# Kernel optimization log

Hardware: AMD Instinct MI355X
Metric: run time of the kernel (lower is better)

The kernel has to match this reference:

```python
import jax, jax.numpy as jnp
import numpy as np

NFEAT, NHID, NCLASS = 256, 128, 40
N_NODES, N_EDGES = 50000, 800000
BN_EPS = 1e-5


def setup_inputs() -> dict:
    key = jax.random.key(0)
    ks = jax.random.split(key, 8)
    x = jax.random.normal(ks[0], (N_NODES, NFEAT), dtype=jnp.float32)
    edge_index = jax.random.randint(ks[1], (2, N_EDGES), 0, N_NODES, dtype=jnp.int64)
    # GCNConv layer 0: nfeat -> nhid (Glorot-ish scale)
    W0 = jax.random.normal(ks[2], (NFEAT, NHID), dtype=jnp.float32) / np.sqrt(NFEAT)
    b0 = jnp.zeros((NHID,), dtype=jnp.float32)
    # BatchNorm1d(nhid)
    gamma0 = jnp.ones((NHID,), dtype=jnp.float32)
    beta0 = jnp.zeros((NHID,), dtype=jnp.float32)
    # GCNConv last: nhid -> nclass
    W1 = jax.random.normal(ks[3], (NHID, NCLASS), dtype=jnp.float32) / np.sqrt(NHID)
    b1 = jnp.zeros((NCLASS,), dtype=jnp.float32)
    return {"x": x, "edge_index": edge_index, "W0": W0, "b0": b0,
            "gamma0": gamma0, "beta0": beta0, "W1": W1, "b1": b1}


def _gcn_conv(x, src, dst, W, b, num_nodes):
    # normalize=False GCNConv: linear transform then raw sum aggregation src->dst
    h = x @ W                                   # [N, out]
    out = jax.ops.segment_sum(h[src], dst, num_segments=num_nodes)
    return out + b


def reference(x, edge_index, W0, b0, gamma0, beta0, W1, b1):
    N = x.shape[0]
    src, dst = edge_index[0], edge_index[1]
    # layer 0 conv
    h = _gcn_conv(x, src, dst, W0, b0, N)       # [N, nhid]
    # BatchNorm1d (training-mode batch stats, biased variance)
    mu = h.mean(axis=0)
    var = jnp.mean((h - mu) ** 2, axis=0)
    h = gamma0 * (h - mu) * jax.lax.rsqrt(var + BN_EPS) + beta0
    h = jax.nn.relu(h)
    # (dropout skipped: deterministic eval baseline)
    # last conv (early-return path in original forward)
    out = _gcn_conv(h, src, dst, W1, b1, N)     # [N, nclass]
    return out
```

## Files before the change

kernel.cpp:

```cpp
#include <hip/hip_runtime.h>

#define NFEAT 256
#define NHID 128
#define NCLASS 40
#define NNODES 50000
#define NEDGES 800000
#define BN_EPS 1e-5f
#define NBK 196
#define NBLK 100
#define EPB 8000
#define BKCAP 6144
#define NW1 6250
#define GEMM1_BLOCKS 1563

typedef __attribute__((ext_vector_type(4))) float f32x4;
typedef __attribute__((ext_vector_type(8))) short bf16x8;

__device__ inline ushort f2bf(float f) {
    uint u = __float_as_uint(f);
    u += 0x7FFF + ((u >> 16) & 1);
    return (ushort)(u >> 16);
}
__device__ inline float bflo(uint v) { return __uint_as_float(v << 16); }
__device__ inline float bfhi(uint v) { return __uint_as_float(v & 0xFFFF0000u); }

__global__ void k_prep(const float* __restrict__ W0, ushort* __restrict__ W0F,
                       const int* __restrict__ ei, int* __restrict__ bcnt) {
    __shared__ int cnt[NBK];
    if (blockIdx.x < 16) {
        const int t = blockIdx.x * 256 + threadIdx.x;
        const int lane = t & 63;
        const int grp = t >> 6;
        const int kc = grp & 7, fi = grp >> 3;
        const int n = fi * 16 + (lane & 15);
        const int k0 = kc * 32 + (lane >> 4) * 8;
        ushort v[8];
        #pragma unroll
        for (int j = 0; j < 8; ++j) v[j] = f2bf(W0[(k0 + j) * NHID + n]);
        uint4 u;
        u.x = (uint)v[0] | ((uint)v[1] << 16);
        u.y = (uint)v[2] | ((uint)v[3] << 16);
        u.z = (uint)v[4] | ((uint)v[5] << 16);
        u.w = (uint)v[6] | ((uint)v[7] << 16);
        *(uint4*)&W0F[(grp * 64 + lane) * 8] = u;
    } else {
        const int blk = blockIdx.x - 16;
        const int t = threadIdx.x;
        if (t < NBK) cnt[t] = 0;
        __syncthreads();
        const int base = blk * EPB;
        for (int i = t; i < EPB; i += 256)
            atomicAdd(&cnt[ei[NEDGES + base + i] >> 8], 1);
        __syncthreads();
        if (t < NBK) bcnt[blk * NBK + t] = cnt[t];
    }
}

__global__ void k_bkscan(const int* __restrict__ bcnt, int* __restrict__ off,
                         int* __restrict__ bstart, int* __restrict__ rowptr,
                         float* __restrict__ stats) {
    __shared__ int tot[NBK];
    __shared__ int bs[NBK + 1];
    const int t = threadIdx.x;
    if (t < 256) stats[t] = 0.f;
    if (t < NBK) {
        int s = 0;
        for (int b = 0; b < NBLK; ++b) s += bcnt[b * NBK + t];
        tot[t] = s;
    }
    __syncthreads();
    if (t == 0) {
        int run = 0;
        for (int i = 0; i < NBK; ++i) { bs[i] = run; run += tot[i]; }
        bs[NBK] = run;
        rowptr[NNODES] = NEDGES;
    }
    __syncthreads();
    if (t <= NBK) bstart[t] = bs[t];
    if (t < NBK) {
        int run = bs[t];
        for (int b = 0; b < NBLK; ++b) { off[b * NBK + t] = run; run += bcnt[b * NBK + t]; }
    }
}

__launch_bounds__(256, 4)
__global__ void k_scatter_gemm1(const int* __restrict__ ei, const int* __restrict__ off,
                                uint* __restrict__ packed,
                                const float* __restrict__ x, const ushort* __restrict__ W0F,
                                ushort* __restrict__ h1) {
    __shared__ int cur[NBK];
    if (blockIdx.x < NBLK) {
        const int t = threadIdx.x, blk = blockIdx.x;
        if (t < NBK) cur[t] = off[blk * NBK + t];
        __syncthreads();
        const int base = blk * EPB;
        for (int i = t; i < EPB; i += 256) {
            const int src = ei[base + i];
            const int dst = ei[NEDGES + base + i];
            const int pos = atomicAdd(&cur[dst >> 8], 1);
            packed[pos] = (uint)src | ((uint)(dst & 255) << 16);
        }
    } else {
        const int gt = (blockIdx.x - NBLK) * 256 + threadIdx.x;
        const int w = gt >> 6;
        if (w >= NW1) return;
        const int lane = gt & 63;
        const int half = w & 1;
        const int node = (w >> 1) * 16 + (lane & 15);
        const int nclamp = node < NNODES ? node : NNODES - 1;
        const float* xg = &x[(long)nclamp * NFEAT + (lane >> 4) * 8];

        bf16x8 xf[8];
        #pragma unroll
        for (int kc = 0; kc < 8; ++kc) {
            const float4 a = *(const float4*)(xg + kc * 32);
            const float4 b = *(const float4*)(xg + kc * 32 + 4);
            xf[kc][0]=(short)f2bf(a.x); xf[kc][1]=(short)f2bf(a.y);
            xf[kc][2]=(short)f2bf(a.z); xf[kc][3]=(short)f2bf(a.w);
            xf[kc][4]=(short)f2bf(b.x); xf[kc][5]=(short)f2bf(b.y);
            xf[kc][6]=(short)f2bf(b.z); xf[kc][7]=(short)f2bf(b.w);
        }

        f32x4 acc[4];
        #pragma unroll
        for (int f = 0; f < 4; ++f) acc[f] = (f32x4){0.f, 0.f, 0.f, 0.f};

        const ushort* wbase = &W0F[(size_t)lane * 8];
        #pragma unroll
        for (int kc = 0; kc < 8; ++kc) {
            #pragma unroll
            for (int f = 0; f < 4; ++f) {
                const int grp = (half * 4 + f) * 8 + kc;
                const bf16x8 wf = *(const bf16x8*)&wbase[(size_t)grp * 64 * 8];
                acc[f] = __builtin_amdgcn_mfma_f32_16x16x32_bf16(wf, xf[kc], acc[f], 0, 0, 0);
            }
        }

        if (node < NNODES) {
            const int nq = (lane >> 4) * 4;
            ushort* hp = &h1[(long)node * NHID + half * 64 + nq];
            #pragma unroll
            for (int f = 0; f < 4; ++f) {
                uint lo = (uint)f2bf(acc[f][0]) | ((uint)f2bf(acc[f][1]) << 16);
                uint hi = (uint)f2bf(acc[f][2]) | ((uint)f2bf(acc[f][3]) << 16);
                *(uint2*)&hp[f * 16] = make_uint2(lo, hi);
            }
        }
    }
}

__launch_bounds__(256)
__global__ void k_bksort(const uint* __restrict__ packed, const int* __restrict__ bstart,
                         int* __restrict__ esrc, int* __restrict__ rowptr) {
    __shared__ uint pr[BKCAP];
    __shared__ int cnt[256], sc[256], cur[256];
    const int t = threadIdx.x, b = blockIdx.x;
    const int nb = bstart[b], ne = bstart[b + 1];
    const int n = ne - nb;
    cnt[t] = 0;
    __syncthreads();
    for (int i = t; i < n; i += 256) {
        const uint p = packed[nb + i];
        pr[i] = p;
        atomicAdd(&cnt[p >> 16], 1);
    }
    __syncthreads();
    const int v = cnt[t];
    sc[t] = v;
    __syncthreads();
    for (int o = 1; o < 256; o <<= 1) {
        const int tmp = (t >= o) ? sc[t - o] : 0;
        __syncthreads();
        sc[t] += tmp;
        __syncthreads();
    }
    const int excl = sc[t] - v;
    cur[t] = excl;
    const int node = (b << 8) + t;
    if (node < NNODES) rowptr[node] = nb + excl;
    __syncthreads();
    for (int i = t; i < n; i += 256) {
        const uint p = pr[i];
        const int pos = atomicAdd(&cur[p >> 16], 1);
        esrc[nb + pos] = (int)(p & 0xFFFFu);
    }
}

__launch_bounds__(256)
__global__ void k_gather1(const int* __restrict__ rowptr, const int* __restrict__ esrc,
                          const ushort* __restrict__ h1, const float* __restrict__ b0,
                          float* __restrict__ agg1) {
    const int w = (blockIdx.x * blockDim.x + threadIdx.x) >> 6;
    const int lane = threadIdx.x & 63;
    if (w >= NNODES) return;
    const int beg = rowptr[w], end = rowptr[w + 1];
    const int f = lane * 2;
    float2 acc = *(const float2*)&b0[f];
    int i = beg;
    for (; i + 7 < end; i += 8) {
        uint v[8];
        #pragma unroll
        for (int j = 0; j < 8; ++j)
            v[j] = *(const uint*)&h1[(long)esrc[i + j] * NHID + f];
        #pragma unroll
        for (int j = 0; j < 8; ++j) { acc.x += bflo(v[j]); acc.y += bfhi(v[j]); }
    }
    for (; i < end; ++i) {
        const uint v = *(const uint*)&h1[(long)esrc[i] * NHID + f];
        acc.x += bflo(v); acc.y += bfhi(v);
    }
    *(float2*)&agg1[(long)w * NHID + f] = acc;
}

__global__ void k_bnstats(const float* __restrict__ agg1,
                          float* __restrict__ sums, float* __restrict__ sumsq) {
    __shared__ float sd[256 * 4], sd2[256 * 4];
    const int t = threadIdx.x;
    const int c4 = (t & 31) * 4;
    const int rr = t >> 5;
    float4 s = make_float4(0.f,0.f,0.f,0.f), s2 = s;
    for (int r = blockIdx.x * 8 + rr; r < NNODES; r += gridDim.x * 8) {
        const float4 v = *(const float4*)&agg1[(long)r * NHID + c4];
        s.x += v.x; s.y += v.y; s.z += v.z; s.w += v.w;
        s2.x += v.x*v.x; s2.y += v.y*v.y; s2.z += v.z*v.z; s2.w += v.w*v.w;
    }
    *(float4*)&sd[t * 4] = s; *(float4*)&sd2[t * 4] = s2;
    __syncthreads();
    if (t < 32) {
        #pragma unroll
        for (int j = 1; j < 8; ++j) {
            const float4 a = *(const float4*)&sd[(j * 32 + t) * 4];
            const float4 a2 = *(const float4*)&sd2[(j * 32 + t) * 4];
            s = *(float4*)&sd[t * 4];
            s2 = *(float4*)&sd2[t * 4];
            s.x += a.x; s.y += a.y; s.z += a.z; s.w += a.w;
            s2.x += a2.x; s2.y += a2.y; s2.z += a2.z; s2.w += a2.w;
            *(float4*)&sd[t * 4] = s; *(float4*)&sd2[t * 4] = s2;
        }
        atomicAdd(&sums[c4 + 0], s.x);  atomicAdd(&sums[c4 + 1], s.y);
        atomicAdd(&sums[c4 + 2], s.z);  atomicAdd(&sums[c4 + 3], s.w);
        atomicAdd(&sumsq[c4 + 0], s2.x); atomicAdd(&sumsq[c4 + 1], s2.y);
        atomicAdd(&sumsq[c4 + 2], s2.z); atomicAdd(&sumsq[c4 + 3], s2.w);
    }
}

__launch_bounds__(256)
__global__ void k_gemm2(const float* __restrict__ agg1, const float* __restrict__ W1,
                        const float* __restrict__ sums, const float* __restrict__ sumsq,
                        const float* __restrict__ gamma, const float* __restrict__ beta,
                        ushort* __restrict__ h2) {
    __shared__ float xs[64 * 132];
    __shared__ float wt[40 * 132];
    __shared__ float s_scale[128], s_shift[128];
    const int t = threadIdx.x;
    const int base = blockIdx.x * 64;

    if (t < NHID) {
        const float mu = sums[t] * (1.f / NNODES);
        float var = sumsq[t] * (1.f / NNODES) - mu * mu;
        var = fmaxf(var, 0.f);
        const float sc = gamma[t] * rsqrtf(var + BN_EPS);
        s_scale[t] = sc;
        s_shift[t] = beta[t] - mu * sc;
    }
    for (int idx = t; idx < NHID * NCLASS; idx += 256) {
        const int c = idx / NCLASS, j = idx % NCLASS;
        wt[j * 132 + c] = W1[idx];
    }
    __syncthreads();
    {
        const int cc = (t & 31) * 4;
        const float4 sc = *(const float4*)&s_scale[cc];
        const float4 sh = *(const float4*)&s_shift[cc];
        const int rb = t >> 5;
        #pragma unroll
        for (int p = 0; p < 8; ++p) {
            const int row = p * 8 + rb;
            const int g = base + row;
            float4 v = make_float4(0.f, 0.f, 0.f, 0.f);
            if (g < NNODES) {
                const float4 a = *(const float4*)&agg1[(long)g * NHID + cc];
                v.x = fmaxf(a.x * sc.x + sh.x, 0.f);
                v.y = fmaxf(a.y * sc.y + sh.y, 0.f);
                v.z = fmaxf(a.z * sc.z + sh.z, 0.f);
                v.w = fmaxf(a.w * sc.w + sh.w, 0.f);
            }
            *(float4*)&xs[row * 132 + cc] = v;
        }
    }
    __syncthreads();

    const int node = t >> 2;
    const int j0 = (t & 3) * 10;
    float acc[10] = {};
    for (int c4 = 0; c4 < 32; ++c4) {
        const int c = c4 * 4;
        const float4 a = *(const float4*)&xs[node * 132 + c];
        #pragma unroll
        for (int jj = 0; jj < 10; ++jj) {
            const float4 wv = *(const float4*)&wt[(j0 + jj) * 132 + c];
            acc[jj] += a.x * wv.x + a.y * wv.y + a.z * wv.z + a.w * wv.w;
        }
    }
    const int g = base + node;
    if (g < NNODES) {
        #pragma unroll
        for (int p = 0; p < 5; ++p) {
            uint u = (uint)f2bf(acc[2 * p]) | ((uint)f2bf(acc[2 * p + 1]) << 16);
            *(uint*)&h2[(long)g * NCLASS + j0 + 2 * p] = u;
        }
    }
}

__launch_bounds__(256)
__global__ void k_gather2(const int* __restrict__ rowptr, const int* __restrict__ esrc,
                          const ushort* __restrict__ h2, const float* __restrict__ b1,
                          float* __restrict__ out) {
    const int t = threadIdx.x;
    if (t >= 240) return;
    const int node = blockIdx.x * 12 + t / 20;
    if (node >= NNODES) return;
    const int f = (t % 20) * 2;
    const int beg = rowptr[node], end = rowptr[node + 1];
    float2 acc = make_float2(b1[f], b1[f + 1]);
    int i = beg;
    for (; i + 3 < end; i += 4) {
        const uint v0 = *(const uint*)&h2[(long)esrc[i]     * NCLASS + f];
        const uint v1 = *(const uint*)&h2[(long)esrc[i + 1] * NCLASS + f];
        const uint v2 = *(const uint*)&h2[(long)esrc[i + 2] * NCLASS + f];
        const uint v3 = *(const uint*)&h2[(long)esrc[i + 3] * NCLASS + f];
        acc.x += (bflo(v0) + bflo(v1)) + (bflo(v2) + bflo(v3));
        acc.y += (bfhi(v0) + bfhi(v1)) + (bfhi(v2) + bfhi(v3));
    }
    for (; i < end; ++i) {
        const uint v = *(const uint*)&h2[(long)esrc[i] * NCLASS + f];
        acc.x += bflo(v); acc.y += bfhi(v);
    }
    *(float2*)&out[(long)node * NCLASS + f] = acc;
}

extern "C" void kernel_launch(void* const* d_in, const int* in_sizes, int n_in,
                              void* d_out, int out_size, void* d_ws, size_t ws_size,
                              hipStream_t stream) {
    const float* x      = (const float*)d_in[0];
    const int*   ei     = (const int*)d_in[1];
    const float* W0     = (const float*)d_in[2];
    const float* b0     = (const float*)d_in[3];
    const float* gamma0 = (const float*)d_in[4];
    const float* beta0  = (const float*)d_in[5];
    const float* W1     = (const float*)d_in[6];
    const float* b1     = (const float*)d_in[7];
    float* out = (float*)d_out;

    char* ws = (char*)d_ws;
    float* sums  = (float*)ws;
    float* sumsq = sums + 128;
    int* wsI     = (int*)(ws + 4096);
    int* rowptr  = wsI;
    int* esrc    = wsI + 50048;
    int* bcnt    = wsI + 850048;
    int* off     = wsI + 869696;
    int* bstart  = wsI + 889344;
    ushort* W0F  = (ushort*)(ws + 3563520);
    ushort* h1   = (ushort*)(ws + 3629056);
    float* agg1  = (float*)(ws + 16429056);
    uint* packed = (uint*)agg1;
    ushort* h2   = h1;

    k_prep<<<16 + NBLK, 256, 0, stream>>>(W0, W0F, ei, bcnt);
    k_bkscan<<<1, 256, 0, stream>>>(bcnt, off, bstart, rowptr, sums);
    k_scatter_gemm1<<<NBLK + GEMM1_BLOCKS, 256, 0, stream>>>(ei, off, packed, x, W0F, h1);
    k_bksort<<<NBK, 256, 0, stream>>>(packed, bstart, esrc, rowptr);
    k_gather1<<<(NNODES * 64 + 255) / 256, 256, 0, stream>>>(rowptr, esrc, h1, b0, agg1);
    k_bnstats<<<256, 256, 0, stream>>>(agg1, sums, sumsq);
    k_gemm2<<<(NNODES + 63) / 64, 256, 0, stream>>>(agg1, W1, sums, sumsq, gamma0, beta0, h2);
    k_gather2<<<(NNODES + 11) / 12, 256, 0, stream>>>(rowptr, esrc, h2, b1, out);
}
```

Baseline: 176.2 us.

## Store layer-1 hidden features as FP8, parallelize bucket scan, batch x loads

The layer-1 hidden features h1 are now stored as packed FP8 e4m3 instead of bf16, which halves the bytes the edge gather reads per edge. The serial bucket prefix sum in k_bkscan is replaced by a parallel shared-memory scan. The GEMM1 path now issues all x loads before converting them, and its launch-bounds occupancy hint is removed. FP8 storage loses precision on the hidden activations, which may push results outside tolerance.

```diff
diff --git a/kernel.cpp b/kernel.cpp
--- a/kernel.cpp
+++ b/kernel.cpp
@@ -1,4 +1,5 @@
 #include <hip/hip_runtime.h>
+#include <hip/hip_fp8.h>
 
 #define NFEAT 256
 #define NHID 128
@@ -24,6 +25,32 @@
 __device__ inline float bflo(uint v) { return __uint_as_float(v << 16); }
 __device__ inline float bfhi(uint v) { return __uint_as_float(v & 0xFFFF0000u); }
 
+__device__ inline uint pk_fp8x4(float a0, float a1, float a2, float a3) {
+#if __has_builtin(__builtin_amdgcn_cvt_pk_fp8_f32)
+    int u = 0;
+    u = __builtin_amdgcn_cvt_pk_fp8_f32(a0, a1, u, false);
+    u = __builtin_amdgcn_cvt_pk_fp8_f32(a2, a3, u, true);
+    return (uint)u;
+#else
+    __hip_fp8_e4m3 q0(a0), q1(a1), q2(a2), q3(a3);
+    return (uint)q0.__x | ((uint)q1.__x << 8) | ((uint)q2.__x << 16) | ((uint)q3.__x << 24);
+#endif
+}
+__device__ inline float fp8lo(uint v) {
+#if __has_builtin(__builtin_amdgcn_cvt_f32_fp8)
+    return __builtin_amdgcn_cvt_f32_fp8((int)v, 0);
+#else
+    __hip_fp8_e4m3 q; q.__x = (__hip_fp8_storage_t)(v & 0xFF); return (float)q;
+#endif
+}
+__device__ inline float fp8hi(uint v) {
+#if __has_builtin(__builtin_amdgcn_cvt_f32_fp8)
+    return __builtin_amdgcn_cvt_f32_fp8((int)v, 1);
+#else
+    __hip_fp8_e4m3 q; q.__x = (__hip_fp8_storage_t)((v >> 8) & 0xFF); return (float)q;
+#endif
+}
+
 __global__ void k_prep(const float* __restrict__ W0, ushort* __restrict__ W0F,
                        const int* __restrict__ ei, int* __restrict__ bcnt) {
     __shared__ int cnt[NBK];
@@ -59,35 +86,35 @@
 __global__ void k_bkscan(const int* __restrict__ bcnt, int* __restrict__ off,
                          int* __restrict__ bstart, int* __restrict__ rowptr,
                          float* __restrict__ stats) {
-    __shared__ int tot[NBK];
-    __shared__ int bs[NBK + 1];
+    __shared__ int sc[256];
     const int t = threadIdx.x;
-    if (t < 256) stats[t] = 0.f;
+    stats[t] = 0.f;
+    int tot = 0;
+    if (t < NBK)
+        for (int b = 0; b < NBLK; ++b) tot += bcnt[b * NBK + t];
+    sc[t] = tot;
+    __syncthreads();
+    for (int o = 1; o < 256; o <<= 1) {
+        const int v = (t >= o) ? sc[t - o] : 0;
+        __syncthreads();
+        sc[t] += v;
+        __syncthreads();
+    }
+    const int excl = sc[t] - tot;
+    if (t < NBK) bstart[t] = excl;
+    else if (t == NBK) bstart[NBK] = sc[NBK - 1];
+    if (t == 0) rowptr[NNODES] = NEDGES;
     if (t < NBK) {
-        int s = 0;
-        for (int b = 0; b < NBLK; ++b) s += bcnt[b * NBK + t];
-        tot[t] = s;
-    }
-    __syncthreads();
-    if (t == 0) {
-        int run = 0;
-        for (int i = 0; i < NBK; ++i) { bs[i] = run; run += tot[i]; }
-        bs[NBK] = run;
-        rowptr[NNODES] = NEDGES;
-    }
-    __syncthreads();
-    if (t <= NBK) bstart[t] = bs[t];
-    if (t < NBK) {
-        int run = bs[t];
+        int run = excl;
         for (int b = 0; b < NBLK; ++b) { off[b * NBK + t] = run; run += bcnt[b * NBK + t]; }
     }
 }
 
-__launch_bounds__(256, 4)
+__launch_bounds__(256)
 __global__ void k_scatter_gemm1(const int* __restrict__ ei, const int* __restrict__ off,
                                 uint* __restrict__ packed,
                                 const float* __restrict__ x, const ushort* __restrict__ W0F,
-                                ushort* __restrict__ h1) {
+                                uchar* __restrict__ h1) {
     __shared__ int cur[NBK];
     if (blockIdx.x < NBLK) {
         const int t = threadIdx.x, blk = blockIdx.x;
@@ -110,21 +137,23 @@
         const int nclamp = node < NNODES ? node : NNODES - 1;
         const float* xg = &x[(long)nclamp * NFEAT + (lane >> 4) * 8];
 
+        float4 xa[8], xb[8];
+        #pragma unroll
+        for (int kc = 0; kc < 8; ++kc) {
+            xa[kc] = *(const float4*)(xg + kc * 32);
+            xb[kc] = *(const float4*)(xg + kc * 32 + 4);
+        }
         bf16x8 xf[8];
         #pragma unroll
         for (int kc = 0; kc < 8; ++kc) {
-            const float4 a = *(const float4*)(xg + kc * 32);
-            const float4 b = *(const float4*)(xg + kc * 32 + 4);
-            xf[kc][0]=(short)f2bf(a.x); xf[kc][1]=(short)f2bf(a.y);
-            xf[kc][2]=(short)f2bf(a.z); xf[kc][3]=(short)f2bf(a.w);
-            xf[kc][4]=(short)f2bf(b.x); xf[kc][5]=(short)f2bf(b.y);
-            xf[kc][6]=(short)f2bf(b.z); xf[kc][7]=(short)f2bf(b.w);
-        }
-
+            xf[kc][0]=(short)f2bf(xa[kc].x); xf[kc][1]=(short)f2bf(xa[kc].y);
+            xf[kc][2]=(short)f2bf(xa[kc].z); xf[kc][3]=(short)f2bf(xa[kc].w);
+            xf[kc][4]=(short)f2bf(xb[kc].x); xf[kc][5]=(short)f2bf(xb[kc].y);
+            xf[kc][6]=(short)f2bf(xb[kc].z); xf[kc][7]=(short)f2bf(xb[kc].w);
+        }
         f32x4 acc[4];
         #pragma unroll
         for (int f = 0; f < 4; ++f) acc[f] = (f32x4){0.f, 0.f, 0.f, 0.f};
-
         const ushort* wbase = &W0F[(size_t)lane * 8];
         #pragma unroll
         for (int kc = 0; kc < 8; ++kc) {
@@ -135,16 +164,12 @@
                 acc[f] = __builtin_amdgcn_mfma_f32_16x16x32_bf16(wf, xf[kc], acc[f], 0, 0, 0);
             }
         }
-
         if (node < NNODES) {
             const int nq = (lane >> 4) * 4;
-            ushort* hp = &h1[(long)node * NHID + half * 64 + nq];
+            uchar* hp = &h1[(long)node * NHID + half * 64 + nq];
             #pragma unroll
-            for (int f = 0; f < 4; ++f) {
-                uint lo = (uint)f2bf(acc[f][0]) | ((uint)f2bf(acc[f][1]) << 16);
-                uint hi = (uint)f2bf(acc[f][2]) | ((uint)f2bf(acc[f][3]) << 16);
-                *(uint2*)&hp[f * 16] = make_uint2(lo, hi);
-            }
+            for (int f = 0; f < 4; ++f)
+                *(uint*)&hp[f * 16] = pk_fp8x4(acc[f][0], acc[f][1], acc[f][2], acc[f][3]);
         }
     }
 }
@@ -188,7 +213,7 @@
 
 __launch_bounds__(256)
 __global__ void k_gather1(const int* __restrict__ rowptr, const int* __restrict__ esrc,
-                          const ushort* __restrict__ h1, const float* __restrict__ b0,
+                          const uchar* __restrict__ h1, const float* __restrict__ b0,
                           float* __restrict__ agg1) {
     const int w = (blockIdx.x * blockDim.x + threadIdx.x) >> 6;
     const int lane = threadIdx.x & 63;
@@ -201,13 +226,13 @@
         uint v[8];
         #pragma unroll
         for (int j = 0; j < 8; ++j)
-            v[j] = *(const uint*)&h1[(long)esrc[i + j] * NHID + f];
-        #pragma unroll
-        for (int j = 0; j < 8; ++j) { acc.x += bflo(v[j]); acc.y += bfhi(v[j]); }
+            v[j] = (uint)*(const ushort*)&h1[(long)esrc[i + j] * NHID + f];
+        #pragma unroll
+        for (int j = 0; j < 8; ++j) { acc.x += fp8lo(v[j]); acc.y += fp8hi(v[j]); }
     }
     for (; i < end; ++i) {
-        const uint v = *(const uint*)&h1[(long)esrc[i] * NHID + f];
-        acc.x += bflo(v); acc.y += bfhi(v);
+        const uint v = (uint)*(const ushort*)&h1[(long)esrc[i] * NHID + f];
+        acc.x += fp8lo(v); acc.y += fp8hi(v);
     }
     *(float2*)&agg1[(long)w * NHID + f] = acc;
 }
@@ -362,10 +387,10 @@
     int* off     = wsI + 869696;
     int* bstart  = wsI + 889344;
     ushort* W0F  = (ushort*)(ws + 3563520);
-    ushort* h1   = (ushort*)(ws + 3629056);
+    uchar* h1    = (uchar*)(ws + 3629056);
     float* agg1  = (float*)(ws + 16429056);
     uint* packed = (uint*)agg1;
-    ushort* h2   = h1;
+    ushort* h2   = (ushort*)h1;
 
     k_prep<<<16 + NBLK, 256, 0, stream>>>(W0, W0F, ei, bcnt);
     k_bkscan<<<1, 256, 0, stream>>>(bcnt, off, bstart, rowptr, sums);
```

Result: faster. 170.3 us (-3.4%).
